# Kernel tuning notes

Measured on AMD Instinct MI355X. Metric: run time of the kernel, lower is better.

Reference implementation:

```python
import jax, jax.numpy as jnp
import numpy as np

B, N_R, N_H, RD, HD = 128, 1, 63, 9, 5
N = N_R + N_H
X_DIM = 128
HID = 64  # wr/wh hidden width
NEG_SLOPE = 0.04
MASK_VAL = -9.0e15


def _glorot(key, shape):
    fan_in, fan_out = shape[0], shape[1]
    lim = jnp.sqrt(6.0 / (fan_in + fan_out))
    return jax.random.uniform(key, shape, jnp.float32, -lim, lim)


def setup_inputs() -> dict:
    key = jax.random.key(0)
    ks = jax.random.split(key, 16)
    d = {
        "robot_state": jax.random.normal(ks[0], (B, N_R, RD), jnp.float32),
        "human_states": jax.random.normal(ks[1], (B, N_H, HD), jnp.float32),
        # w_r: Linear(9->64) ReLU Linear(64->128) ReLU
        "wr_W1": _glorot(ks[2], (RD, HID)), "wr_b1": jnp.zeros((HID,), jnp.float32),
        "wr_W2": _glorot(ks[3], (HID, X_DIM)), "wr_b2": jnp.zeros((X_DIM,), jnp.float32),
        # w_h: Linear(5->64) ReLU Linear(64->128) ReLU
        "wh_W1": _glorot(ks[4], (HD, HID)), "wh_b1": jnp.zeros((HID,), jnp.float32),
        "wh_W2": _glorot(ks[5], (HID, X_DIM)), "wh_b2": jnp.zeros((X_DIM,), jnp.float32),
        # gat0.w_a: Linear(256->256) ReLU Linear(256->1)
        "g0_W1": _glorot(ks[6], (2 * X_DIM, 2 * X_DIM)), "g0_b1": jnp.zeros((2 * X_DIM,), jnp.float32),
        "g0_W2": _glorot(ks[7], (2 * X_DIM, 1)), "g0_b2": jnp.zeros((1,), jnp.float32),
        # gat1.w_a
        "g1_W1": _glorot(ks[8], (2 * X_DIM, 2 * X_DIM)), "g1_b1": jnp.zeros((2 * X_DIM,), jnp.float32),
        "g1_W2": _glorot(ks[9], (2 * X_DIM, 1)), "g1_b2": jnp.zeros((1,), jnp.float32),
    }
    return d


def _mlp2(x, W1, b1, W2, b2, last_relu):
    h = jax.nn.relu(x @ W1 + b1)
    y = h @ W2 + b2
    return jax.nn.relu(y) if last_relu else y


def _gat_layer(X, adj, W1, b1, W2, b2):
    # X: [B, N, D]; pairwise features [B, N, N, 2D] (row i = source, col j = target)
    b, n, d = X.shape
    Pi = jnp.broadcast_to(X[:, :, None, :], (b, n, n, d))
    Pj = jnp.broadcast_to(X[:, None, :, :], (b, n, n, d))
    pair = jnp.concatenate([Pi, Pj], axis=-1)            # [B,N,N,2D]
    A = _mlp2(pair, W1, b1, W2, b2, last_relu=False)[..., 0]  # [B,N,N]
    e = jnp.where(A > 0, A, NEG_SLOPE * A)               # LeakyReLU(0.04)
    masked = jnp.where(adj > 0, e, MASK_VAL)
    attn = jax.nn.softmax(masked, axis=2)
    return jnp.matmul(attn, X)                            # [B,N,D]


def reference(robot_state, human_states,
              wr_W1, wr_b1, wr_W2, wr_b2,
              wh_W1, wh_b1, wh_W2, wh_b2,
              g0_W1, g0_b1, g0_W2, g0_b2,
              g1_W1, g1_b1, g1_W2, g1_b2):
    # adjacency: all-ones except humans cannot attend to robot (col 0)
    adj = jnp.ones((N, N), jnp.float32).at[N_R:, 0].set(0.0)
    adj = jnp.broadcast_to(adj, (robot_state.shape[0], N, N))
    r_emb = _mlp2(robot_state, wr_W1, wr_b1, wr_W2, wr_b2, last_relu=True)
    h_emb = _mlp2(human_states, wh_W1, wh_b1, wh_W2, wh_b2, last_relu=True)
    X = jnp.concatenate([r_emb, h_emb], axis=1)           # [B,N,X_DIM]
    H1 = _gat_layer(X, adj, g0_W1, g0_b1, g0_W2, g0_b2)
    H2 = _gat_layer(H1, adj, g1_W1, g1_b1, g1_W2, g1_b2)
    return H1 + H2 + X  # skip_connection=True
```

## Files before the change

### kernel.cpp

```cpp
#include <hip/hip_runtime.h>

#define NEG_SLOPE 0.04f
#define MASK_VAL  -9.0e15f

namespace {
constexpr int Bz   = 128;
constexpr int NN   = 64;
constexpr int RDim = 9;
constexpr int HDim = 5;
constexpr int HIDv = 64;
constexpr int XDv  = 128;
}

__global__ __launch_bounds__(256) void embed_kernel(
    const float* __restrict__ robot, const float* __restrict__ human,
    const float* __restrict__ wrW1, const float* __restrict__ wrb1,
    const float* __restrict__ wrW2, const float* __restrict__ wrb2,
    const float* __restrict__ whW1, const float* __restrict__ whb1,
    const float* __restrict__ whW2, const float* __restrict__ whb2,
    float* __restrict__ X)
{
  __shared__ float hs[16 * HIDv];
  const int b  = blockIdx.x >> 2;
  const int rg = blockIdx.x & 3;
  const int t  = threadIdx.x;

  for (int v = t; v < 16 * HIDv; v += 256) {
    const int nl = v >> 6, k = v & 63;
    const int n  = rg * 16 + nl;
    const float* W1; const float* b1; const float* in; int K;
    if (n == 0) { W1 = wrW1; b1 = wrb1; in = robot + b * RDim;                K = RDim; }
    else        { W1 = whW1; b1 = whb1; in = human + (b * 63 + n - 1) * HDim; K = HDim; }
    float acc = b1[k];
    for (int j = 0; j < K; ++j) acc = fmaf(in[j], W1[j * HIDv + k], acc);
    hs[v] = fmaxf(acc, 0.f);
  }
  __syncthreads();

  const int d     = t & 127;
  const int which = t >> 7;

  float acc[8];
#pragma unroll
  for (int c = 0; c < 8; ++c) acc[c] = whb2[d];

  for (int k4 = 0; k4 < 16; ++k4) {
    float w4[4];
#pragma unroll
    for (int kk = 0; kk < 4; ++kk) w4[kk] = whW2[(4 * k4 + kk) * XDv + d];
#pragma unroll
    for (int c = 0; c < 8; ++c) {
      const float4 h4 = *reinterpret_cast<const float4*>(&hs[(2 * c + which) * HIDv + 4 * k4]);
      acc[c] = fmaf(h4.x, w4[0], acc[c]);
      acc[c] = fmaf(h4.y, w4[1], acc[c]);
      acc[c] = fmaf(h4.z, w4[2], acc[c]);
      acc[c] = fmaf(h4.w, w4[3], acc[c]);
    }
  }
  if (rg == 0 && which == 0) {
    float a = wrb2[d];
#pragma unroll 8
    for (int k = 0; k < HIDv; ++k) a = fmaf(hs[k], wrW2[k * XDv + d], a);
    acc[0] = a;
  }
#pragma unroll
  for (int c = 0; c < 8; ++c) {
    const int n = rg * 16 + 2 * c + which;
    X[(size_t)(b * NN + n) * XDv + d] = fmaxf(acc[c], 0.f);
  }
}

__global__ __launch_bounds__(256) void transform_kernel(
    const float* __restrict__ Xin, const float* __restrict__ W1,
    const float* __restrict__ b1, float* __restrict__ UV)
{
  __shared__ float Xs[16 * XDv];
  const int t = threadIdx.x;
  const int base = blockIdx.x * 16;

  for (int idx = t; idx < 16 * XDv / 4; idx += 256)
    *reinterpret_cast<float4*>(Xs + idx * 4) =
        *reinterpret_cast<const float4*>(Xin + (size_t)base * XDv + idx * 4);
  __syncthreads();

  float acc0[16], acc1[16];
  const float bias = b1[t];
#pragma unroll
  for (int n = 0; n < 16; ++n) { acc0[n] = bias; acc1[n] = 0.f; }

  for (int k = 0; k < XDv; k += 4) {
    float w0[4], w1[4];
#pragma unroll
    for (int kk = 0; kk < 4; ++kk) {
      w0[kk] = W1[(k + kk) * 256 + t];
      w1[kk] = W1[(128 + k + kk) * 256 + t];
    }
#pragma unroll
    for (int n = 0; n < 16; ++n) {
      const float4 x4 = *reinterpret_cast<const float4*>(&Xs[n * XDv + k]);
      acc0[n] = fmaf(x4.x, w0[0], acc0[n]);
      acc0[n] = fmaf(x4.y, w0[1], acc0[n]);
      acc0[n] = fmaf(x4.z, w0[2], acc0[n]);
      acc0[n] = fmaf(x4.w, w0[3], acc0[n]);
      acc1[n] = fmaf(x4.x, w1[0], acc1[n]);
      acc1[n] = fmaf(x4.y, w1[1], acc1[n]);
      acc1[n] = fmaf(x4.z, w1[2], acc1[n]);
      acc1[n] = fmaf(x4.w, w1[3], acc1[n]);
    }
  }
#pragma unroll
  for (int n = 0; n < 16; ++n) {
    UV[(size_t)(base + n) * 512 + t]       = acc0[n];
    UV[(size_t)(base + n) * 512 + 256 + t] = acc1[n];
  }
}

__global__ __launch_bounds__(256) void attn_kernel(
    const float* __restrict__ UV, const float* __restrict__ Xpv,
    const float* __restrict__ Xskip, const float* __restrict__ W2g,
    const float* __restrict__ b2g, float* __restrict__ out, int add_skip)
{
  __shared__ float smem[16384];
  float* Vsf = smem;

  const int b  = blockIdx.x >> 2;
  const int rg = blockIdx.x & 3;
  const int t  = threadIdx.x;
  const float* UVb = UV + (size_t)b * NN * 512;

  for (int cc = t; cc < NN * 64; cc += 256) {
    const int j = cc >> 6, c = cc & 63;
    const float4 v = *reinterpret_cast<const float4*>(UVb + j * 512 + 256 + (c << 2));
    *reinterpret_cast<float4*>(Vsf + j * 256 + ((c ^ (j & 7)) << 2)) = v;
  }
  __syncthreads();

  const int wv = t >> 6;
  const int lane = t & 63;
  const int jx = lane & 7;

  float e[4] = {0.f, 0.f, 0.f, 0.f};
  const float* Up[4];
#pragma unroll
  for (int q = 0; q < 4; ++q)
    Up[q] = UVb + (size_t)(rg * 16 + 4 * wv + q) * 512;

#pragma unroll 2
  for (int c = 0; c < 64; ++c) {
    const float4 v4 = *reinterpret_cast<const float4*>(Vsf + lane * 256 + ((c ^ jx) << 2));
    const float4 w4 = *reinterpret_cast<const float4*>(W2g + (c << 2));
#pragma unroll
    for (int q = 0; q < 4; ++q) {
      const float4 u4 = *reinterpret_cast<const float4*>(Up[q] + (c << 2));
      e[q] = fmaf(fmaxf(u4.x + v4.x, 0.f), w4.x, e[q]);
      e[q] = fmaf(fmaxf(u4.y + v4.y, 0.f), w4.y, e[q]);
      e[q] = fmaf(fmaxf(u4.z + v4.z, 0.f), w4.z, e[q]);
      e[q] = fmaf(fmaxf(u4.w + v4.w, 0.f), w4.w, e[q]);
    }
  }

  const float bias2 = b2g[0];
  float att[4];
#pragma unroll
  for (int q = 0; q < 4; ++q) {
    float s = e[q] + bias2;
    s = s > 0.f ? s : NEG_SLOPE * s;
    const int i_glob = rg * 16 + 4 * wv + q;
    if (i_glob > 0 && lane == 0) s = MASK_VAL;
    float m = s;
#pragma unroll
    for (int off = 32; off > 0; off >>= 1) m = fmaxf(m, __shfl_xor(m, off));
    const float p = __expf(s - m);
    float sum = p;
#pragma unroll
    for (int off = 32; off > 0; off >>= 1) sum += __shfl_xor(sum, off);
    att[q] = p / sum;
  }
  __syncthreads();

  float* Xs = smem;
  float* As = smem + 8192;
#pragma unroll
  for (int q = 0; q < 4; ++q) As[(4 * wv + q) * 64 + lane] = att[q];

  const float* Xb = Xpv + (size_t)b * NN * XDv;
  for (int idx = t; idx < NN * XDv / 4; idx += 256)
    *reinterpret_cast<float4*>(Xs + idx * 4) =
        *reinterpret_cast<const float4*>(Xb + idx * 4);
  __syncthreads();

  const int l32 = t & 31, grp = t >> 5;
  const int d4 = l32 << 2;
  float4 a0 = {0.f, 0.f, 0.f, 0.f}, a1 = {0.f, 0.f, 0.f, 0.f};
  for (int j = 0; j < NN; ++j) {
    const float4 x4 = *reinterpret_cast<const float4*>(Xs + j * XDv + d4);
    const float w0 = As[grp * 64 + j];
    const float w1 = As[(grp + 8) * 64 + j];
    a0.x = fmaf(w0, x4.x, a0.x); a0.y = fmaf(w0, x4.y, a0.y);
    a0.z = fmaf(w0, x4.z, a0.z); a0.w = fmaf(w0, x4.w, a0.w);
    a1.x = fmaf(w1, x4.x, a1.x); a1.y = fmaf(w1, x4.y, a1.y);
    a1.z = fmaf(w1, x4.z, a1.z); a1.w = fmaf(w1, x4.w, a1.w);
  }

  const int i0 = rg * 16 + grp, i1 = rg * 16 + grp + 8;
  if (add_skip) {
    const float4 h0 = *reinterpret_cast<const float4*>(Xs + i0 * XDv + d4);
    const float4 h1 = *reinterpret_cast<const float4*>(Xs + i1 * XDv + d4);
    const float4 s0 = *reinterpret_cast<const float4*>(Xskip + ((size_t)b * NN + i0) * XDv + d4);
    const float4 s1 = *reinterpret_cast<const float4*>(Xskip + ((size_t)b * NN + i1) * XDv + d4);
    a0.x += h0.x + s0.x; a0.y += h0.y + s0.y; a0.z += h0.z + s0.z; a0.w += h0.w + s0.w;
    a1.x += h1.x + s1.x; a1.y += h1.y + s1.y; a1.z += h1.z + s1.z; a1.w += h1.w + s1.w;
  }
  *reinterpret_cast<float4*>(out + ((size_t)b * NN + i0) * XDv + d4) = a0;
  *reinterpret_cast<float4*>(out + ((size_t)b * NN + i1) * XDv + d4) = a1;
}

extern "C" void kernel_launch(void* const* d_in, const int* in_sizes, int n_in,
                              void* d_out, int out_size, void* d_ws, size_t ws_size,
                              hipStream_t stream) {
  const float* robot = (const float*)d_in[0];
  const float* human = (const float*)d_in[1];
  const float* wrW1  = (const float*)d_in[2];
  const float* wrb1  = (const float*)d_in[3];
  const float* wrW2  = (const float*)d_in[4];
  const float* wrb2  = (const float*)d_in[5];
  const float* whW1  = (const float*)d_in[6];
  const float* whb1  = (const float*)d_in[7];
  const float* whW2  = (const float*)d_in[8];
  const float* whb2  = (const float*)d_in[9];
  const float* g0W1  = (const float*)d_in[10];
  const float* g0b1  = (const float*)d_in[11];
  const float* g0W2  = (const float*)d_in[12];
  const float* g0b2  = (const float*)d_in[13];
  const float* g1W1  = (const float*)d_in[14];
  const float* g1b1  = (const float*)d_in[15];
  const float* g1W2  = (const float*)d_in[16];
  const float* g1b2  = (const float*)d_in[17];
  float* out = (float*)d_out;

  float* X   = (float*)d_ws;
  float* H1  = X  + (size_t)Bz * NN * XDv;
  float* UVb = H1 + (size_t)Bz * NN * XDv;

  embed_kernel<<<Bz * 4, 256, 0, stream>>>(robot, human, wrW1, wrb1, wrW2, wrb2,
                                           whW1, whb1, whW2, whb2, X);
  transform_kernel<<<Bz * NN / 16, 256, 0, stream>>>(X, g0W1, g0b1, UVb);
  attn_kernel<<<Bz * 4, 256, 0, stream>>>(UVb, X, nullptr, g0W2, g0b2, H1, 0);
  transform_kernel<<<Bz * NN / 16, 256, 0, stream>>>(H1, g1W1, g1b1, UVb);
  attn_kernel<<<Bz * 4, 256, 0, stream>>>(UVb, H1, X, g1W2, g1b2, out, 1);
}
```

Measured before the change: 207.0 us.

## Fuse embedding, transform and attention into two per-layer kernels

Replaces five launches (embed, two transforms, two attention passes) with two 512-thread kernels, one per GAT layer, each handling half a batch's rows. The U and V projections are computed in shared memory instead of being written to and re-read from a global UV buffer, which removes that round trip and three launches. In exchange, each half-block recomputes the full V projection for all 64 nodes, and layer 1 also recomputes the embedding for the whole batch. The kernels use 128 KB of shared memory, which limits residency to one block per CU, and only 256 blocks are launched.

```diff
diff --git a/kernel.cpp b/kernel.cpp
--- a/kernel.cpp
+++ b/kernel.cpp
@@ -4,215 +4,254 @@
 #define MASK_VAL  -9.0e15f
 
 namespace {
-constexpr int Bz   = 128;
-constexpr int NN   = 64;
-constexpr int RDim = 9;
-constexpr int HDim = 5;
-constexpr int HIDv = 64;
-constexpr int XDv  = 128;
-}
-
-__global__ __launch_bounds__(256) void embed_kernel(
+constexpr int Bz = 128;
+constexpr int NN = 64;
+constexpr int XD = 128;
+constexpr int HID = 64;
+}
+
+__device__ __forceinline__ void gat_layer(
+    const float* __restrict__ Ns, float* __restrict__ Vs, float* __restrict__ UsAs,
+    const float* __restrict__ W1, const float* __restrict__ b1,
+    const float* __restrict__ W2, const float* __restrict__ b2,
+    int h, int t, float4& o0, float4& o1)
+{
+  const int w = t >> 6, l = t & 63;
+
+  {
+    float vac[8][4];
+#pragma unroll
+    for (int nn = 0; nn < 8; ++nn)
+#pragma unroll
+      for (int c = 0; c < 4; ++c) vac[nn][c] = 0.f;
+
+    for (int ks = 0; ks < XD; ks += 4) {
+      float wr[4][4];
+#pragma unroll
+      for (int kk = 0; kk < 4; ++kk) {
+        const float4 wv = *reinterpret_cast<const float4*>(&W1[(XD + ks + kk) * 256 + (l << 2)]);
+        wr[kk][0] = wv.x; wr[kk][1] = wv.y; wr[kk][2] = wv.z; wr[kk][3] = wv.w;
+      }
+#pragma unroll
+      for (int nn = 0; nn < 8; ++nn) {
+        const float4 x4 = *reinterpret_cast<const float4*>(&Ns[(8 * w + nn) * XD + ks]);
+        const float xk0 = x4.x, xk1 = x4.y, xk2 = x4.z, xk3 = x4.w;
+#pragma unroll
+        for (int c = 0; c < 4; ++c) {
+          vac[nn][c] = fmaf(xk0, wr[0][c], vac[nn][c]);
+          vac[nn][c] = fmaf(xk1, wr[1][c], vac[nn][c]);
+          vac[nn][c] = fmaf(xk2, wr[2][c], vac[nn][c]);
+          vac[nn][c] = fmaf(xk3, wr[3][c], vac[nn][c]);
+        }
+      }
+    }
+#pragma unroll
+    for (int nn = 0; nn < 8; ++nn) {
+      const int n = 8 * w + nn;
+      const float4 v = {vac[nn][0], vac[nn][1], vac[nn][2], vac[nn][3]};
+      *reinterpret_cast<float4*>(&Vs[n * 256 + ((l ^ (n & 7)) << 2)]) = v;
+    }
+  }
+
+  {
+    float uac[4][4];
+    const float4 bi = *reinterpret_cast<const float4*>(&b1[l << 2]);
+#pragma unroll
+    for (int q = 0; q < 4; ++q) { uac[q][0] = bi.x; uac[q][1] = bi.y; uac[q][2] = bi.z; uac[q][3] = bi.w; }
+
+    for (int ks = 0; ks < XD; ks += 4) {
+      float wr[4][4];
+#pragma unroll
+      for (int kk = 0; kk < 4; ++kk) {
+        const float4 wv = *reinterpret_cast<const float4*>(&W1[(ks + kk) * 256 + (l << 2)]);
+        wr[kk][0] = wv.x; wr[kk][1] = wv.y; wr[kk][2] = wv.z; wr[kk][3] = wv.w;
+      }
+#pragma unroll
+      for (int q = 0; q < 4; ++q) {
+        const float4 x4 = *reinterpret_cast<const float4*>(&Ns[(32 * h + 4 * w + q) * XD + ks]);
+        const float xk0 = x4.x, xk1 = x4.y, xk2 = x4.z, xk3 = x4.w;
+#pragma unroll
+        for (int c = 0; c < 4; ++c) {
+          uac[q][c] = fmaf(xk0, wr[0][c], uac[q][c]);
+          uac[q][c] = fmaf(xk1, wr[1][c], uac[q][c]);
+          uac[q][c] = fmaf(xk2, wr[2][c], uac[q][c]);
+          uac[q][c] = fmaf(xk3, wr[3][c], uac[q][c]);
+        }
+      }
+    }
+#pragma unroll
+    for (int q = 0; q < 4; ++q) {
+      const float4 u = {uac[q][0], uac[q][1], uac[q][2], uac[q][3]};
+      *reinterpret_cast<float4*>(&UsAs[(4 * w + q) * 256 + (l << 2)]) = u;
+    }
+  }
+  __syncthreads();
+
+  float att[4];
+  {
+    const int jx = l & 7;
+    float e[4] = {0.f, 0.f, 0.f, 0.f};
+    for (int c4 = 0; c4 < 64; ++c4) {
+      const float4 v4 = *reinterpret_cast<const float4*>(&Vs[l * 256 + ((c4 ^ jx) << 2)]);
+      const float4 w4 = *reinterpret_cast<const float4*>(&W2[c4 << 2]);
+#pragma unroll
+      for (int q = 0; q < 4; ++q) {
+        const float4 u4 = *reinterpret_cast<const float4*>(&UsAs[(4 * w + q) * 256 + (c4 << 2)]);
+        e[q] = fmaf(fmaxf(u4.x + v4.x, 0.f), w4.x, e[q]);
+        e[q] = fmaf(fmaxf(u4.y + v4.y, 0.f), w4.y, e[q]);
+        e[q] = fmaf(fmaxf(u4.z + v4.z, 0.f), w4.z, e[q]);
+        e[q] = fmaf(fmaxf(u4.w + v4.w, 0.f), w4.w, e[q]);
+      }
+    }
+    const float bias2 = b2[0];
+#pragma unroll
+    for (int q = 0; q < 4; ++q) {
+      float s = e[q] + bias2;
+      s = s > 0.f ? s : NEG_SLOPE * s;
+      const int gi = 32 * h + 4 * w + q;
+      if (gi > 0 && l == 0) s = MASK_VAL;
+      float m = s;
+#pragma unroll
+      for (int off = 32; off > 0; off >>= 1) m = fmaxf(m, __shfl_xor(m, off));
+      const float p = __expf(s - m);
+      float sum = p;
+#pragma unroll
+      for (int off = 32; off > 0; off >>= 1) sum += __shfl_xor(sum, off);
+      att[q] = p / sum;
+    }
+  }
+  __syncthreads();
+#pragma unroll
+  for (int q = 0; q < 4; ++q) UsAs[(4 * w + q) * 64 + l] = att[q];
+  __syncthreads();
+
+  {
+    const int grp = t >> 5, d4 = (t & 31) << 2;
+    float4 a0 = {0.f, 0.f, 0.f, 0.f}, a1 = {0.f, 0.f, 0.f, 0.f};
+    for (int j = 0; j < NN; ++j) {
+      const float4 x4 = *reinterpret_cast<const float4*>(&Ns[j * XD + d4]);
+      const float wA = UsAs[grp * 64 + j];
+      const float wB = UsAs[(grp + 16) * 64 + j];
+      a0.x = fmaf(wA, x4.x, a0.x); a0.y = fmaf(wA, x4.y, a0.y);
+      a0.z = fmaf(wA, x4.z, a0.z); a0.w = fmaf(wA, x4.w, a0.w);
+      a1.x = fmaf(wB, x4.x, a1.x); a1.y = fmaf(wB, x4.y, a1.y);
+      a1.z = fmaf(wB, x4.z, a1.z); a1.w = fmaf(wB, x4.w, a1.w);
+    }
+    o0 = a0; o1 = a1;
+  }
+}
+
+__global__ __launch_bounds__(512) void layer1_kernel(
     const float* __restrict__ robot, const float* __restrict__ human,
     const float* __restrict__ wrW1, const float* __restrict__ wrb1,
     const float* __restrict__ wrW2, const float* __restrict__ wrb2,
     const float* __restrict__ whW1, const float* __restrict__ whb1,
     const float* __restrict__ whW2, const float* __restrict__ whb2,
-    float* __restrict__ X)
+    const float* __restrict__ W1, const float* __restrict__ b1,
+    const float* __restrict__ W2, const float* __restrict__ b2,
+    float* __restrict__ Xg, float* __restrict__ H1g)
 {
-  __shared__ float hs[16 * HIDv];
-  const int b  = blockIdx.x >> 2;
-  const int rg = blockIdx.x & 3;
-  const int t  = threadIdx.x;
-
-  for (int v = t; v < 16 * HIDv; v += 256) {
-    const int nl = v >> 6, k = v & 63;
-    const int n  = rg * 16 + nl;
-    const float* W1; const float* b1; const float* in; int K;
-    if (n == 0) { W1 = wrW1; b1 = wrb1; in = robot + b * RDim;                K = RDim; }
-    else        { W1 = whW1; b1 = whb1; in = human + (b * 63 + n - 1) * HDim; K = HDim; }
-    float acc = b1[k];
-    for (int j = 0; j < K; ++j) acc = fmaf(in[j], W1[j * HIDv + k], acc);
+  __shared__ float smem[32768];
+  float* Xs = smem;
+  float* Vs = smem + 8192;
+  float* Us = smem + 24576;
+  float* hs = smem + 24576;
+
+  const int b = blockIdx.x >> 1, h = blockIdx.x & 1;
+  const int t = threadIdx.x;
+
+  for (int v = t; v < NN * HID; v += 512) {
+    const int n = v >> 6, k = v & 63;
+    float acc;
+    if (n == 0) {
+      acc = wrb1[k];
+      for (int j = 0; j < 9; ++j) acc = fmaf(robot[b * 9 + j], wrW1[j * HID + k], acc);
+    } else {
+      const float* in = human + (b * 63 + n - 1) * 5;
+      acc = whb1[k];
+      for (int j = 0; j < 5; ++j) acc = fmaf(in[j], whW1[j * HID + k], acc);
+    }
     hs[v] = fmaxf(acc, 0.f);
   }
   __syncthreads();
 
-  const int d     = t & 127;
-  const int which = t >> 7;
-
-  float acc[8];
-#pragma unroll
-  for (int c = 0; c < 8; ++c) acc[c] = whb2[d];
-
-  for (int k4 = 0; k4 < 16; ++k4) {
-    float w4[4];
-#pragma unroll
-    for (int kk = 0; kk < 4; ++kk) w4[kk] = whW2[(4 * k4 + kk) * XDv + d];
-#pragma unroll
-    for (int c = 0; c < 8; ++c) {
-      const float4 h4 = *reinterpret_cast<const float4*>(&hs[(2 * c + which) * HIDv + 4 * k4]);
-      acc[c] = fmaf(h4.x, w4[0], acc[c]);
-      acc[c] = fmaf(h4.y, w4[1], acc[c]);
-      acc[c] = fmaf(h4.z, w4[2], acc[c]);
-      acc[c] = fmaf(h4.w, w4[3], acc[c]);
-    }
-  }
-  if (rg == 0 && which == 0) {
-    float a = wrb2[d];
+  {
+    const int d = t & 127, which = t >> 7;
+    float xacc[16];
+#pragma unroll
+    for (int c = 0; c < 16; ++c) xacc[c] = whb2[d];
+
+    for (int k4 = 0; k4 < 16; ++k4) {
+      float w4[4];
+#pragma unroll
+      for (int kk = 0; kk < 4; ++kk) w4[kk] = whW2[(4 * k4 + kk) * XD + d];
+#pragma unroll
+      for (int c = 0; c < 16; ++c) {
+        const float4 h4 = *reinterpret_cast<const float4*>(&hs[(4 * c + which) * HID + 4 * k4]);
+        xacc[c] = fmaf(h4.x, w4[0], xacc[c]);
+        xacc[c] = fmaf(h4.y, w4[1], xacc[c]);
+        xacc[c] = fmaf(h4.z, w4[2], xacc[c]);
+        xacc[c] = fmaf(h4.w, w4[3], xacc[c]);
+      }
+    }
+    if (which == 0) {
+      float a = wrb2[d];
 #pragma unroll 8
-    for (int k = 0; k < HIDv; ++k) a = fmaf(hs[k], wrW2[k * XDv + d], a);
-    acc[0] = a;
-  }
-#pragma unroll
-  for (int c = 0; c < 8; ++c) {
-    const int n = rg * 16 + 2 * c + which;
-    X[(size_t)(b * NN + n) * XDv + d] = fmaxf(acc[c], 0.f);
-  }
-}
-
-__global__ __launch_bounds__(256) void transform_kernel(
-    const float* __restrict__ Xin, const float* __restrict__ W1,
-    const float* __restrict__ b1, float* __restrict__ UV)
+      for (int k = 0; k < HID; ++k) a = fmaf(hs[k], wrW2[k * XD + d], a);
+      xacc[0] = a;
+    }
+#pragma unroll
+    for (int c = 0; c < 16; ++c) {
+      const int n = 4 * c + which;
+      const float val = fmaxf(xacc[c], 0.f);
+      Xs[n * XD + d] = val;
+      if ((n >> 5) == h) Xg[((size_t)(b * NN + n)) * XD + d] = val;
+    }
+  }
+  __syncthreads();
+
+  float4 a0, a1;
+  gat_layer(Xs, Vs, Us, W1, b1, W2, b2, h, t, a0, a1);
+
+  const int grp = t >> 5, d4 = (t & 31) << 2;
+  const int n0 = 32 * h + grp, n1 = n0 + 16;
+  *reinterpret_cast<float4*>(&H1g[((size_t)(b * NN + n0)) * XD + d4]) = a0;
+  *reinterpret_cast<float4*>(&H1g[((size_t)(b * NN + n1)) * XD + d4]) = a1;
+}
+
+__global__ __launch_bounds__(512) void layer2_kernel(
+    const float* __restrict__ H1g, const float* __restrict__ Xg,
+    const float* __restrict__ W1, const float* __restrict__ b1,
+    const float* __restrict__ W2, const float* __restrict__ b2,
+    float* __restrict__ out)
 {
-  __shared__ float Xs[16 * XDv];
+  __shared__ float smem[32768];
+  float* Ys = smem;
+  float* Vs = smem + 8192;
+  float* Us = smem + 24576;
+
+  const int b = blockIdx.x >> 1, h = blockIdx.x & 1;
   const int t = threadIdx.x;
-  const int base = blockIdx.x * 16;
-
-  for (int idx = t; idx < 16 * XDv / 4; idx += 256)
-    *reinterpret_cast<float4*>(Xs + idx * 4) =
-        *reinterpret_cast<const float4*>(Xin + (size_t)base * XDv + idx * 4);
-  __syncthreads();
-
-  float acc0[16], acc1[16];
-  const float bias = b1[t];
-#pragma unroll
-  for (int n = 0; n < 16; ++n) { acc0[n] = bias; acc1[n] = 0.f; }
-
-  for (int k = 0; k < XDv; k += 4) {
-    float w0[4], w1[4];
-#pragma unroll
-    for (int kk = 0; kk < 4; ++kk) {
-      w0[kk] = W1[(k + kk) * 256 + t];
-      w1[kk] = W1[(128 + k + kk) * 256 + t];
-    }
-#pragma unroll
-    for (int n = 0; n < 16; ++n) {
-      const float4 x4 = *reinterpret_cast<const float4*>(&Xs[n * XDv + k]);
-      acc0[n] = fmaf(x4.x, w0[0], acc0[n]);
-      acc0[n] = fmaf(x4.y, w0[1], acc0[n]);
-      acc0[n] = fmaf(x4.z, w0[2], acc0[n]);
-      acc0[n] = fmaf(x4.w, w0[3], acc0[n]);
-      acc1[n] = fmaf(x4.x, w1[0], acc1[n]);
-      acc1[n] = fmaf(x4.y, w1[1], acc1[n]);
-      acc1[n] = fmaf(x4.z, w1[2], acc1[n]);
-      acc1[n] = fmaf(x4.w, w1[3], acc1[n]);
-    }
-  }
-#pragma unroll
-  for (int n = 0; n < 16; ++n) {
-    UV[(size_t)(base + n) * 512 + t]       = acc0[n];
-    UV[(size_t)(base + n) * 512 + 256 + t] = acc1[n];
-  }
-}
-
-__global__ __launch_bounds__(256) void attn_kernel(
-    const float* __restrict__ UV, const float* __restrict__ Xpv,
-    const float* __restrict__ Xskip, const float* __restrict__ W2g,
-    const float* __restrict__ b2g, float* __restrict__ out, int add_skip)
-{
-  __shared__ float smem[16384];
-  float* Vsf = smem;
-
-  const int b  = blockIdx.x >> 2;
-  const int rg = blockIdx.x & 3;
-  const int t  = threadIdx.x;
-  const float* UVb = UV + (size_t)b * NN * 512;
-
-  for (int cc = t; cc < NN * 64; cc += 256) {
-    const int j = cc >> 6, c = cc & 63;
-    const float4 v = *reinterpret_cast<const float4*>(UVb + j * 512 + 256 + (c << 2));
-    *reinterpret_cast<float4*>(Vsf + j * 256 + ((c ^ (j & 7)) << 2)) = v;
-  }
-  __syncthreads();
-
-  const int wv = t >> 6;
-  const int lane = t & 63;
-  const int jx = lane & 7;
-
-  float e[4] = {0.f, 0.f, 0.f, 0.f};
-  const float* Up[4];
-#pragma unroll
-  for (int q = 0; q < 4; ++q)
-    Up[q] = UVb + (size_t)(rg * 16 + 4 * wv + q) * 512;
-
-#pragma unroll 2
-  for (int c = 0; c < 64; ++c) {
-    const float4 v4 = *reinterpret_cast<const float4*>(Vsf + lane * 256 + ((c ^ jx) << 2));
-    const float4 w4 = *reinterpret_cast<const float4*>(W2g + (c << 2));
-#pragma unroll
-    for (int q = 0; q < 4; ++q) {
-      const float4 u4 = *reinterpret_cast<const float4*>(Up[q] + (c << 2));
-      e[q] = fmaf(fmaxf(u4.x + v4.x, 0.f), w4.x, e[q]);
-      e[q] = fmaf(fmaxf(u4.y + v4.y, 0.f), w4.y, e[q]);
-      e[q] = fmaf(fmaxf(u4.z + v4.z, 0.f), w4.z, e[q]);
-      e[q] = fmaf(fmaxf(u4.w + v4.w, 0.f), w4.w, e[q]);
-    }
-  }
-
-  const float bias2 = b2g[0];
-  float att[4];
-#pragma unroll
-  for (int q = 0; q < 4; ++q) {
-    float s = e[q] + bias2;
-    s = s > 0.f ? s : NEG_SLOPE * s;
-    const int i_glob = rg * 16 + 4 * wv + q;
-    if (i_glob > 0 && lane == 0) s = MASK_VAL;
-    float m = s;
-#pragma unroll
-    for (int off = 32; off > 0; off >>= 1) m = fmaxf(m, __shfl_xor(m, off));
-    const float p = __expf(s - m);
-    float sum = p;
-#pragma unroll
-    for (int off = 32; off > 0; off >>= 1) sum += __shfl_xor(sum, off);
-    att[q] = p / sum;
-  }
-  __syncthreads();
-
-  float* Xs = smem;
-  float* As = smem + 8192;
-#pragma unroll
-  for (int q = 0; q < 4; ++q) As[(4 * wv + q) * 64 + lane] = att[q];
-
-  const float* Xb = Xpv + (size_t)b * NN * XDv;
-  for (int idx = t; idx < NN * XDv / 4; idx += 256)
-    *reinterpret_cast<float4*>(Xs + idx * 4) =
-        *reinterpret_cast<const float4*>(Xb + idx * 4);
-  __syncthreads();
-
-  const int l32 = t & 31, grp = t >> 5;
-  const int d4 = l32 << 2;
-  float4 a0 = {0.f, 0.f, 0.f, 0.f}, a1 = {0.f, 0.f, 0.f, 0.f};
-  for (int j = 0; j < NN; ++j) {
-    const float4 x4 = *reinterpret_cast<const float4*>(Xs + j * XDv + d4);
-    const float w0 = As[grp * 64 + j];
-    const float w1 = As[(grp + 8) * 64 + j];
-    a0.x = fmaf(w0, x4.x, a0.x); a0.y = fmaf(w0, x4.y, a0.y);
-    a0.z = fmaf(w0, x4.z, a0.z); a0.w = fmaf(w0, x4.w, a0.w);
-    a1.x = fmaf(w1, x4.x, a1.x); a1.y = fmaf(w1, x4.y, a1.y);
-    a1.z = fmaf(w1, x4.z, a1.z); a1.w = fmaf(w1, x4.w, a1.w);
-  }
-
-  const int i0 = rg * 16 + grp, i1 = rg * 16 + grp + 8;
-  if (add_skip) {
-    const float4 h0 = *reinterpret_cast<const float4*>(Xs + i0 * XDv + d4);
-    const float4 h1 = *reinterpret_cast<const float4*>(Xs + i1 * XDv + d4);
-    const float4 s0 = *reinterpret_cast<const float4*>(Xskip + ((size_t)b * NN + i0) * XDv + d4);
-    const float4 s1 = *reinterpret_cast<const float4*>(Xskip + ((size_t)b * NN + i1) * XDv + d4);
-    a0.x += h0.x + s0.x; a0.y += h0.y + s0.y; a0.z += h0.z + s0.z; a0.w += h0.w + s0.w;
-    a1.x += h1.x + s1.x; a1.y += h1.y + s1.y; a1.z += h1.z + s1.z; a1.w += h1.w + s1.w;
-  }
-  *reinterpret_cast<float4*>(out + ((size_t)b * NN + i0) * XDv + d4) = a0;
-  *reinterpret_cast<float4*>(out + ((size_t)b * NN + i1) * XDv + d4) = a1;
+
+  const float* Hb = H1g + (size_t)b * NN * XD;
+  for (int idx = t; idx < NN * XD / 4; idx += 512)
+    *reinterpret_cast<float4*>(Ys + idx * 4) =
+        *reinterpret_cast<const float4*>(Hb + idx * 4);
+  __syncthreads();
+
+  float4 a0, a1;
+  gat_layer(Ys, Vs, Us, W1, b1, W2, b2, h, t, a0, a1);
+
+  const int grp = t >> 5, d4 = (t & 31) << 2;
+  const int n0 = 32 * h + grp, n1 = n0 + 16;
+  const float4 y0 = *reinterpret_cast<const float4*>(&Ys[n0 * XD + d4]);
+  const float4 y1 = *reinterpret_cast<const float4*>(&Ys[n1 * XD + d4]);
+  const float4 x0 = *reinterpret_cast<const float4*>(&Xg[((size_t)(b * NN + n0)) * XD + d4]);
+  const float4 x1 = *reinterpret_cast<const float4*>(&Xg[((size_t)(b * NN + n1)) * XD + d4]);
+  a0.x += y0.x + x0.x; a0.y += y0.y + x0.y; a0.z += y0.z + x0.z; a0.w += y0.w + x0.w;
+  a1.x += y1.x + x1.x; a1.y += y1.y + x1.y; a1.z += y1.z + x1.z; a1.w += y1.w + x1.w;
+  *reinterpret_cast<float4*>(&out[((size_t)(b * NN + n0)) * XD + d4]) = a0;
+  *reinterpret_cast<float4*>(&out[((size_t)(b * NN + n1)) * XD + d4]) = a1;
 }
 
 extern "C" void kernel_launch(void* const* d_in, const int* in_sizes, int n_in,
@@ -238,14 +277,11 @@
   const float* g1b2  = (const float*)d_in[17];
   float* out = (float*)d_out;
 
-  float* X   = (float*)d_ws;
-  float* H1  = X  + (size_t)Bz * NN * XDv;
-  float* UVb = H1 + (size_t)Bz * NN * XDv;
-
-  embed_kernel<<<Bz * 4, 256, 0, stream>>>(robot, human, wrW1, wrb1, wrW2, wrb2,
-                                           whW1, whb1, whW2, whb2, X);
-  transform_kernel<<<Bz * NN / 16, 256, 0, stream>>>(X, g0W1, g0b1, UVb);
-  attn_kernel<<<Bz * 4, 256, 0, stream>>>(UVb, X, nullptr, g0W2, g0b2, H1, 0);
-  transform_kernel<<<Bz * NN / 16, 256, 0, stream>>>(H1, g1W1, g1b1, UVb);
-  attn_kernel<<<Bz * 4, 256, 0, stream>>>(UVb, H1, X, g1W2, g1b2, out, 1);
-}
+  float* Xg  = (float*)d_ws;
+  float* H1g = Xg + (size_t)Bz * NN * XD;
+
+  layer1_kernel<<<Bz * 2, 512, 0, stream>>>(robot, human, wrW1, wrb1, wrW2, wrb2,
+                                            whW1, whb1, whW2, whb2,
+                                            g0W1, g0b1, g0W2, g0b2, Xg, H1g);
+  layer2_kernel<<<Bz * 2, 512, 0, stream>>>(H1g, Xg, g1W1, g1b1, g1W2, g1b2, out);
+}
```

Measured after the change: 174.1 us. -15.9%, faster.

## Fuse U-projection into attention kernel and split V transform

Applied to the files above, without the earlier changes.

The transform kernel now computes only the V half (target features) of the first GAT linear layer into a 256-wide buffer. The U half for each block's own rows is computed inside the attention kernel, with bias, and broadcast across lanes via readlane. This removes the U write and read through global memory. The attention kernel moves to 512 threads with two rows per wave, stages W2 in shared memory, and reads X for aggregation directly from global memory rather than staging it. The cost is extra per-block weight reads from W1 and heavier register use in the attention kernel.

```diff
diff --git a/kernel.cpp b/kernel.cpp
--- a/kernel.cpp
+++ b/kernel.cpp
@@ -3,13 +3,19 @@
 #define NEG_SLOPE 0.04f
 #define MASK_VAL  -9.0e15f
 
+#define FMA4(acc, s, w4) \
+  acc.x = fmaf(s, w4.x, acc.x); acc.y = fmaf(s, w4.y, acc.y); \
+  acc.z = fmaf(s, w4.z, acc.z); acc.w = fmaf(s, w4.w, acc.w)
+
 namespace {
-constexpr int Bz   = 128;
-constexpr int NN   = 64;
-constexpr int RDim = 9;
-constexpr int HDim = 5;
-constexpr int HIDv = 64;
-constexpr int XDv  = 128;
+constexpr int Bz = 128;
+constexpr int NN = 64;
+constexpr int XD = 128;
+constexpr int HID = 64;
+}
+
+__device__ __forceinline__ float rl_f(float v, int lane) {
+  return __int_as_float(__builtin_amdgcn_readlane(__float_as_int(v), lane));
 }
 
 __global__ __launch_bounds__(256) void embed_kernel(
@@ -20,26 +26,28 @@
     const float* __restrict__ whW2, const float* __restrict__ whb2,
     float* __restrict__ X)
 {
-  __shared__ float hs[16 * HIDv];
+  __shared__ float hs[16 * HID];
   const int b  = blockIdx.x >> 2;
   const int rg = blockIdx.x & 3;
   const int t  = threadIdx.x;
 
-  for (int v = t; v < 16 * HIDv; v += 256) {
+  for (int v = t; v < 16 * HID; v += 256) {
     const int nl = v >> 6, k = v & 63;
     const int n  = rg * 16 + nl;
-    const float* W1; const float* b1; const float* in; int K;
-    if (n == 0) { W1 = wrW1; b1 = wrb1; in = robot + b * RDim;                K = RDim; }
-    else        { W1 = whW1; b1 = whb1; in = human + (b * 63 + n - 1) * HDim; K = HDim; }
-    float acc = b1[k];
-    for (int j = 0; j < K; ++j) acc = fmaf(in[j], W1[j * HIDv + k], acc);
+    float acc;
+    if (n == 0) {
+      acc = wrb1[k];
+      for (int j = 0; j < 9; ++j) acc = fmaf(robot[b * 9 + j], wrW1[j * HID + k], acc);
+    } else {
+      const float* in = human + (b * 63 + n - 1) * 5;
+      acc = whb1[k];
+      for (int j = 0; j < 5; ++j) acc = fmaf(in[j], whW1[j * HID + k], acc);
+    }
     hs[v] = fmaxf(acc, 0.f);
   }
   __syncthreads();
 
-  const int d     = t & 127;
-  const int which = t >> 7;
-
+  const int d = t & 127, which = t >> 7;
   float acc[8];
 #pragma unroll
   for (int c = 0; c < 8; ++c) acc[c] = whb2[d];
@@ -47,10 +55,10 @@
   for (int k4 = 0; k4 < 16; ++k4) {
     float w4[4];
 #pragma unroll
-    for (int kk = 0; kk < 4; ++kk) w4[kk] = whW2[(4 * k4 + kk) * XDv + d];
+    for (int kk = 0; kk < 4; ++kk) w4[kk] = whW2[(4 * k4 + kk) * XD + d];
 #pragma unroll
     for (int c = 0; c < 8; ++c) {
-      const float4 h4 = *reinterpret_cast<const float4*>(&hs[(2 * c + which) * HIDv + 4 * k4]);
+      const float4 h4 = *reinterpret_cast<const float4*>(&hs[(2 * c + which) * HID + 4 * k4]);
       acc[c] = fmaf(h4.x, w4[0], acc[c]);
       acc[c] = fmaf(h4.y, w4[1], acc[c]);
       acc[c] = fmaf(h4.z, w4[2], acc[c]);
@@ -60,159 +68,164 @@
   if (rg == 0 && which == 0) {
     float a = wrb2[d];
 #pragma unroll 8
-    for (int k = 0; k < HIDv; ++k) a = fmaf(hs[k], wrW2[k * XDv + d], a);
+    for (int k = 0; k < HID; ++k) a = fmaf(hs[k], wrW2[k * XD + d], a);
     acc[0] = a;
   }
 #pragma unroll
   for (int c = 0; c < 8; ++c) {
     const int n = rg * 16 + 2 * c + which;
-    X[(size_t)(b * NN + n) * XDv + d] = fmaxf(acc[c], 0.f);
-  }
-}
-
-__global__ __launch_bounds__(256) void transform_kernel(
+    X[(size_t)(b * NN + n) * XD + d] = fmaxf(acc[c], 0.f);
+  }
+}
+
+__global__ __launch_bounds__(256) void vtrans_kernel(
     const float* __restrict__ Xin, const float* __restrict__ W1,
-    const float* __restrict__ b1, float* __restrict__ UV)
+    float* __restrict__ Vg)
 {
-  __shared__ float Xs[16 * XDv];
+  __shared__ float Xs[8 * XD];
   const int t = threadIdx.x;
-  const int base = blockIdx.x * 16;
-
-  for (int idx = t; idx < 16 * XDv / 4; idx += 256)
-    *reinterpret_cast<float4*>(Xs + idx * 4) =
-        *reinterpret_cast<const float4*>(Xin + (size_t)base * XDv + idx * 4);
-  __syncthreads();
-
-  float acc0[16], acc1[16];
-  const float bias = b1[t];
-#pragma unroll
-  for (int n = 0; n < 16; ++n) { acc0[n] = bias; acc1[n] = 0.f; }
-
-  for (int k = 0; k < XDv; k += 4) {
-    float w0[4], w1[4];
-#pragma unroll
-    for (int kk = 0; kk < 4; ++kk) {
-      w0[kk] = W1[(k + kk) * 256 + t];
-      w1[kk] = W1[(128 + k + kk) * 256 + t];
-    }
-#pragma unroll
-    for (int n = 0; n < 16; ++n) {
-      const float4 x4 = *reinterpret_cast<const float4*>(&Xs[n * XDv + k]);
-      acc0[n] = fmaf(x4.x, w0[0], acc0[n]);
-      acc0[n] = fmaf(x4.y, w0[1], acc0[n]);
-      acc0[n] = fmaf(x4.z, w0[2], acc0[n]);
-      acc0[n] = fmaf(x4.w, w0[3], acc0[n]);
-      acc1[n] = fmaf(x4.x, w1[0], acc1[n]);
-      acc1[n] = fmaf(x4.y, w1[1], acc1[n]);
-      acc1[n] = fmaf(x4.z, w1[2], acc1[n]);
-      acc1[n] = fmaf(x4.w, w1[3], acc1[n]);
-    }
-  }
-#pragma unroll
-  for (int n = 0; n < 16; ++n) {
-    UV[(size_t)(base + n) * 512 + t]       = acc0[n];
-    UV[(size_t)(base + n) * 512 + 256 + t] = acc1[n];
-  }
-}
-
-__global__ __launch_bounds__(256) void attn_kernel(
-    const float* __restrict__ UV, const float* __restrict__ Xpv,
-    const float* __restrict__ Xskip, const float* __restrict__ W2g,
-    const float* __restrict__ b2g, float* __restrict__ out, int add_skip)
+  const int base = blockIdx.x * 8;
+  reinterpret_cast<float4*>(Xs)[t] =
+      reinterpret_cast<const float4*>(Xin + (size_t)base * XD)[t];
+  __syncthreads();
+
+  float acc[8];
+#pragma unroll
+  for (int n = 0; n < 8; ++n) acc[n] = 0.f;
+  for (int k = 0; k < XD; k += 4) {
+    const float w0 = W1[(XD + k    ) * 256 + t];
+    const float w1 = W1[(XD + k + 1) * 256 + t];
+    const float w2 = W1[(XD + k + 2) * 256 + t];
+    const float w3 = W1[(XD + k + 3) * 256 + t];
+#pragma unroll
+    for (int n = 0; n < 8; ++n) {
+      const float4 x4 = *reinterpret_cast<const float4*>(&Xs[n * XD + k]);
+      acc[n] = fmaf(x4.x, w0, acc[n]);
+      acc[n] = fmaf(x4.y, w1, acc[n]);
+      acc[n] = fmaf(x4.z, w2, acc[n]);
+      acc[n] = fmaf(x4.w, w3, acc[n]);
+    }
+  }
+#pragma unroll
+  for (int n = 0; n < 8; ++n)
+    Vg[(size_t)(base + n) * 256 + t] = acc[n];
+}
+
+__global__ __launch_bounds__(512, 4) void attn_kernel(
+    const float* __restrict__ Vg, const float* __restrict__ Xu,
+    const float* __restrict__ Xskip,
+    const float* __restrict__ W1, const float* __restrict__ b1,
+    const float* __restrict__ W2g, const float* __restrict__ b2g,
+    float* __restrict__ out, int add_skip)
 {
-  __shared__ float smem[16384];
-  float* Vsf = smem;
+  __shared__ float smem[17664];
+  float* Vs  = smem;
+  float* As  = smem + 16384;
+  float* W2s = smem + 17408;
 
   const int b  = blockIdx.x >> 2;
   const int rg = blockIdx.x & 3;
   const int t  = threadIdx.x;
-  const float* UVb = UV + (size_t)b * NN * 512;
-
-  for (int cc = t; cc < NN * 64; cc += 256) {
+  const int w  = t >> 6, l = t & 63;
+
+  const float* Vb = Vg + (size_t)b * NN * 256;
+  for (int cc = t; cc < NN * 64; cc += 512) {
     const int j = cc >> 6, c = cc & 63;
-    const float4 v = *reinterpret_cast<const float4*>(UVb + j * 512 + 256 + (c << 2));
-    *reinterpret_cast<float4*>(Vsf + j * 256 + ((c ^ (j & 7)) << 2)) = v;
-  }
-  __syncthreads();
-
-  const int wv = t >> 6;
-  const int lane = t & 63;
-  const int jx = lane & 7;
-
-  float e[4] = {0.f, 0.f, 0.f, 0.f};
-  const float* Up[4];
-#pragma unroll
-  for (int q = 0; q < 4; ++q)
-    Up[q] = UVb + (size_t)(rg * 16 + 4 * wv + q) * 512;
-
+    const float4 v = *reinterpret_cast<const float4*>(Vb + j * 256 + (c << 2));
+    *reinterpret_cast<float4*>(Vs + j * 256 + ((c ^ (j & 7)) << 2)) = v;
+  }
+  if (t < 64)
+    reinterpret_cast<float4*>(W2s)[t] = reinterpret_cast<const float4*>(W2g)[t];
+
+  float4 ua0, ua1;
+  {
+    const float4 bi = *reinterpret_cast<const float4*>(&b1[l << 2]);
+    ua0 = bi; ua1 = bi;
+    const float* x0 = Xu + (size_t)(b * NN + rg * 16 + 2 * w) * XD;
+    const float* x1 = x0 + XD;
 #pragma unroll 2
-  for (int c = 0; c < 64; ++c) {
-    const float4 v4 = *reinterpret_cast<const float4*>(Vsf + lane * 256 + ((c ^ jx) << 2));
-    const float4 w4 = *reinterpret_cast<const float4*>(W2g + (c << 2));
-#pragma unroll
-    for (int q = 0; q < 4; ++q) {
-      const float4 u4 = *reinterpret_cast<const float4*>(Up[q] + (c << 2));
-      e[q] = fmaf(fmaxf(u4.x + v4.x, 0.f), w4.x, e[q]);
-      e[q] = fmaf(fmaxf(u4.y + v4.y, 0.f), w4.y, e[q]);
-      e[q] = fmaf(fmaxf(u4.z + v4.z, 0.f), w4.z, e[q]);
-      e[q] = fmaf(fmaxf(u4.w + v4.w, 0.f), w4.w, e[q]);
-    }
-  }
-
-  const float bias2 = b2g[0];
-  float att[4];
-#pragma unroll
-  for (int q = 0; q < 4; ++q) {
-    float s = e[q] + bias2;
-    s = s > 0.f ? s : NEG_SLOPE * s;
-    const int i_glob = rg * 16 + 4 * wv + q;
-    if (i_glob > 0 && lane == 0) s = MASK_VAL;
-    float m = s;
-#pragma unroll
-    for (int off = 32; off > 0; off >>= 1) m = fmaxf(m, __shfl_xor(m, off));
-    const float p = __expf(s - m);
-    float sum = p;
-#pragma unroll
-    for (int off = 32; off > 0; off >>= 1) sum += __shfl_xor(sum, off);
-    att[q] = p / sum;
-  }
-  __syncthreads();
-
-  float* Xs = smem;
-  float* As = smem + 8192;
-#pragma unroll
-  for (int q = 0; q < 4; ++q) As[(4 * wv + q) * 64 + lane] = att[q];
-
-  const float* Xb = Xpv + (size_t)b * NN * XDv;
-  for (int idx = t; idx < NN * XDv / 4; idx += 256)
-    *reinterpret_cast<float4*>(Xs + idx * 4) =
-        *reinterpret_cast<const float4*>(Xb + idx * 4);
-  __syncthreads();
-
-  const int l32 = t & 31, grp = t >> 5;
-  const int d4 = l32 << 2;
-  float4 a0 = {0.f, 0.f, 0.f, 0.f}, a1 = {0.f, 0.f, 0.f, 0.f};
+    for (int ks = 0; ks < XD; ks += 4) {
+      const float4 wu0 = *reinterpret_cast<const float4*>(&W1[(ks    ) * 256 + (l << 2)]);
+      const float4 wu1 = *reinterpret_cast<const float4*>(&W1[(ks + 1) * 256 + (l << 2)]);
+      const float4 wu2 = *reinterpret_cast<const float4*>(&W1[(ks + 2) * 256 + (l << 2)]);
+      const float4 wu3 = *reinterpret_cast<const float4*>(&W1[(ks + 3) * 256 + (l << 2)]);
+      const float4 xa = *reinterpret_cast<const float4*>(&x0[ks]);
+      const float4 xb = *reinterpret_cast<const float4*>(&x1[ks]);
+      FMA4(ua0, xa.x, wu0); FMA4(ua0, xa.y, wu1); FMA4(ua0, xa.z, wu2); FMA4(ua0, xa.w, wu3);
+      FMA4(ua1, xb.x, wu0); FMA4(ua1, xb.y, wu1); FMA4(ua1, xb.z, wu2); FMA4(ua1, xb.w, wu3);
+    }
+  }
+  __syncthreads();
+
+  float att0, att1;
+  {
+    const int jx = l & 7;
+    float e0 = 0.f, e1 = 0.f;
+    for (int c4 = 0; c4 < 64; ++c4) {
+      const float4 v4 = *reinterpret_cast<const float4*>(&Vs[l * 256 + ((c4 ^ jx) << 2)]);
+      const float4 w4 = *reinterpret_cast<const float4*>(&W2s[c4 << 2]);
+      const float4 u0 = make_float4(rl_f(ua0.x, c4), rl_f(ua0.y, c4),
+                                    rl_f(ua0.z, c4), rl_f(ua0.w, c4));
+      const float4 u1 = make_float4(rl_f(ua1.x, c4), rl_f(ua1.y, c4),
+                                    rl_f(ua1.z, c4), rl_f(ua1.w, c4));
+      e0 = fmaf(fmaxf(u0.x + v4.x, 0.f), w4.x, e0);
+      e0 = fmaf(fmaxf(u0.y + v4.y, 0.f), w4.y, e0);
+      e0 = fmaf(fmaxf(u0.z + v4.z, 0.f), w4.z, e0);
+      e0 = fmaf(fmaxf(u0.w + v4.w, 0.f), w4.w, e0);
+      e1 = fmaf(fmaxf(u1.x + v4.x, 0.f), w4.x, e1);
+      e1 = fmaf(fmaxf(u1.y + v4.y, 0.f), w4.y, e1);
+      e1 = fmaf(fmaxf(u1.z + v4.z, 0.f), w4.z, e1);
+      e1 = fmaf(fmaxf(u1.w + v4.w, 0.f), w4.w, e1);
+    }
+    const float bias2 = b2g[0];
+    const int gi0 = rg * 16 + 2 * w;
+    {
+      float s = e0 + bias2;
+      s = s > 0.f ? s : NEG_SLOPE * s;
+      if (gi0 > 0 && l == 0) s = MASK_VAL;
+      float m = s;
+#pragma unroll
+      for (int off = 32; off > 0; off >>= 1) m = fmaxf(m, __shfl_xor(m, off));
+      const float p = __expf(s - m);
+      float sum = p;
+#pragma unroll
+      for (int off = 32; off > 0; off >>= 1) sum += __shfl_xor(sum, off);
+      att0 = p / sum;
+    }
+    {
+      float s = e1 + bias2;
+      s = s > 0.f ? s : NEG_SLOPE * s;
+      if (l == 0) s = MASK_VAL;
+      float m = s;
+#pragma unroll
+      for (int off = 32; off > 0; off >>= 1) m = fmaxf(m, __shfl_xor(m, off));
+      const float p = __expf(s - m);
+      float sum = p;
+#pragma unroll
+      for (int off = 32; off > 0; off >>= 1) sum += __shfl_xor(sum, off);
+      att1 = p / sum;
+    }
+  }
+  As[(2 * w) * 64 + l]     = att0;
+  As[(2 * w + 1) * 64 + l] = att1;
+  __syncthreads();
+
+  const int grp = t >> 5, d4 = (t & 31) << 2;
+  const int row = rg * 16 + grp;
+  float4 a = {0.f, 0.f, 0.f, 0.f};
+  const float* Xb = Xu + (size_t)b * NN * XD;
+#pragma unroll 4
   for (int j = 0; j < NN; ++j) {
-    const float4 x4 = *reinterpret_cast<const float4*>(Xs + j * XDv + d4);
-    const float w0 = As[grp * 64 + j];
-    const float w1 = As[(grp + 8) * 64 + j];
-    a0.x = fmaf(w0, x4.x, a0.x); a0.y = fmaf(w0, x4.y, a0.y);
-    a0.z = fmaf(w0, x4.z, a0.z); a0.w = fmaf(w0, x4.w, a0.w);
-    a1.x = fmaf(w1, x4.x, a1.x); a1.y = fmaf(w1, x4.y, a1.y);
-    a1.z = fmaf(w1, x4.z, a1.z); a1.w = fmaf(w1, x4.w, a1.w);
-  }
-
-  const int i0 = rg * 16 + grp, i1 = rg * 16 + grp + 8;
+    const float4 x4 = *reinterpret_cast<const float4*>(&Xb[j * XD + d4]);
+    const float wA = As[grp * 64 + j];
+    FMA4(a, wA, x4);
+  }
   if (add_skip) {
-    const float4 h0 = *reinterpret_cast<const float4*>(Xs + i0 * XDv + d4);
-    const float4 h1 = *reinterpret_cast<const float4*>(Xs + i1 * XDv + d4);
-    const float4 s0 = *reinterpret_cast<const float4*>(Xskip + ((size_t)b * NN + i0) * XDv + d4);
-    const float4 s1 = *reinterpret_cast<const float4*>(Xskip + ((size_t)b * NN + i1) * XDv + d4);
-    a0.x += h0.x + s0.x; a0.y += h0.y + s0.y; a0.z += h0.z + s0.z; a0.w += h0.w + s0.w;
-    a1.x += h1.x + s1.x; a1.y += h1.y + s1.y; a1.z += h1.z + s1.z; a1.w += h1.w + s1.w;
-  }
-  *reinterpret_cast<float4*>(out + ((size_t)b * NN + i0) * XDv + d4) = a0;
-  *reinterpret_cast<float4*>(out + ((size_t)b * NN + i1) * XDv + d4) = a1;
+    const float4 h1 = *reinterpret_cast<const float4*>(&Xb[row * XD + d4]);
+    const float4 x0 = *reinterpret_cast<const float4*>(&Xskip[((size_t)(b * NN + row)) * XD + d4]);
+    a.x += h1.x + x0.x; a.y += h1.y + x0.y; a.z += h1.z + x0.z; a.w += h1.w + x0.w;
+  }
+  *reinterpret_cast<float4*>(&out[((size_t)(b * NN + row)) * XD + d4]) = a;
 }
 
 extern "C" void kernel_launch(void* const* d_in, const int* in_sizes, int n_in,
@@ -238,14 +251,16 @@
   const float* g1b2  = (const float*)d_in[17];
   float* out = (float*)d_out;
 
-  float* X   = (float*)d_ws;
-  float* H1  = X  + (size_t)Bz * NN * XDv;
-  float* UVb = H1 + (size_t)Bz * NN * XDv;
+  float* Xg  = (float*)d_ws;
+  float* H1g = Xg  + (size_t)Bz * NN * XD;
+  float* Vg  = H1g + (size_t)Bz * NN * XD;
 
   embed_kernel<<<Bz * 4, 256, 0, stream>>>(robot, human, wrW1, wrb1, wrW2, wrb2,
-                                           whW1, whb1, whW2, whb2, X);
-  transform_kernel<<<Bz * NN / 16, 256, 0, stream>>>(X, g0W1, g0b1, UVb);
-  attn_kernel<<<Bz * 4, 256, 0, stream>>>(UVb, X, nullptr, g0W2, g0b2, H1, 0);
-  transform_kernel<<<Bz * NN / 16, 256, 0, stream>>>(H1, g1W1, g1b1, UVb);
-  attn_kernel<<<Bz * 4, 256, 0, stream>>>(UVb, H1, X, g1W2, g1b2, out, 1);
-}
+                                           whW1, whb1, whW2, whb2, Xg);
+  vtrans_kernel<<<Bz * NN / 8, 256, 0, stream>>>(Xg, g0W1, Vg);
+  attn_kernel<<<Bz * 4, 512, 0, stream>>>(Vg, Xg, nullptr,
+                                          g0W1, g0b1, g0W2, g0b2, H1g, 0);
+  vtrans_kernel<<<Bz * NN / 8, 256, 0, stream>>>(H1g, g1W1, Vg);
+  attn_kernel<<<Bz * 4, 512, 0, stream>>>(Vg, H1g, Xg,
+                                          g1W1, g1b1, g1W2, g1b2, out, 1);
+}
```

Measured after the change: 229.1 us. 10.7% more time.
